# Kernel tuning notes

Hardware: AMD Instinct MI355X
Metric: run time of the kernel (lower is better)

The kernel has to match this reference:

```python
import jax, jax.numpy as jnp
import numpy as np

LN_EPS = 1e-5

def _ln(x, w, b):
    mu = jnp.mean(x, -1, keepdims=True)
    var = jnp.mean((x - mu) ** 2, -1, keepdims=True)
    return (x - mu) / jnp.sqrt(var + LN_EPS) * w + b

def _rot_fwd(x, c, s):
    dh = x.shape[-1] // 2
    r, i = x[..., :dh], x[..., dh:]
    return jnp.concatenate([r * c - i * s, r * s + i * c], axis=-1)

def _rot_inv(x, c, s):
    dh = x.shape[-1] // 2
    r, i = x[..., :dh], x[..., dh:]
    return jnp.concatenate([r * c + i * s, -r * s + i * c], axis=-1)

def _sheaf(x, thetas, alpha, corr_W):
    # causal offsets for window=3
    B, T, d = x.shape
    offsets = [-3, -2, -1, 0]
    lap = jnp.zeros_like(x)
    for idx, delta in enumerate(offsets):
        th = thetas[idx]
        c, s = jnp.cos(th), jnp.sin(th)
        Rx = _rot_fwd(x, c, s)
        if delta == 0:
            x_nb = x
        else:
            ad = -delta
            zeros = jnp.zeros((B, ad, d), dtype=x.dtype)
            x_nb = jnp.concatenate([zeros, x[:, :T - ad, :]], axis=1)
        lap = lap + _rot_inv(Rx - x_nb, c, s)
    out = x - jnp.abs(alpha) * lap
    return out + jnp.einsum('btd,od->bto', out, corr_W)

def _gist_rotation(x, gist_theta, gist_mag, gist_weights, gist_strength, ln_w, ln_b):
    # Scale-1 path: gist_weights present. theta: (B, dh)
    dh = x.shape[-1] // 2
    w = gist_weights[..., None] * gist_mag              # (B, K, 1)
    w = w / (jnp.sum(w, axis=1, keepdims=True) + 1e-8)
    theta = jnp.sum(w * gist_theta, axis=1)             # (B, dh)
    theta = theta * jax.nn.sigmoid(gist_strength)
    c = jnp.cos(theta)[:, None, :]                      # (B, 1, dh)
    s = jnp.sin(theta)[:, None, :]
    r, i = x[..., :dh], x[..., dh:]
    rot = jnp.concatenate([r * c - i * s, r * s + i * c], axis=-1)
    return _ln(rot, ln_w, ln_b)

def _gist_cross_attn(x, gist_theta, gist_mag, Wq, Wk, Wv, Wo, gist_up_W, gist_up_b, n_heads=16):
    B, T, d = x.shape
    K = gist_theta.shape[1]
    dh = d // n_heads
    gist_repr = jnp.einsum('bkf,of->bko', jnp.concatenate([gist_theta, gist_mag], axis=-1), gist_up_W) + gist_up_b  # (B,K,d)
    Q = jnp.einsum('btd,od->bto', x, Wq).reshape(B, T, n_heads, dh).transpose(0, 2, 1, 3)          # (B,H,T,dh)
    Kh = jnp.einsum('bkd,od->bko', gist_repr, Wk).reshape(B, K, n_heads, dh).transpose(0, 2, 1, 3)  # (B,H,K,dh)
    V = jnp.einsum('bkd,od->bko', gist_repr, Wv).reshape(B, K, n_heads, dh).transpose(0, 2, 1, 3)
    scores = jnp.einsum('bhtd,bhkd->bhtk', Q, Kh) / jnp.sqrt(jnp.asarray(dh, x.dtype))
    ctx = jnp.einsum('bhtk,bhkd->bhtd', jax.nn.softmax(scores, axis=-1), V)
    ctx = ctx.transpose(0, 2, 1, 3).reshape(B, T, d)
    return jnp.einsum('btd,od->bto', ctx, Wo)

def _forward(x, gist_theta, gist_mag, gist_weights,
             ln_sheaf_w, ln_sheaf_b, sheaf_thetas, alpha, corr_W,
             ln_gist_w, ln_gist_b, gist_strength, gr_ln_w, gr_ln_b,
             ln_gca_w, ln_gca_b, Wq, Wk, Wv, Wo, gist_up_W, gist_up_b):
    x = x + _sheaf(_ln(x, ln_sheaf_w, ln_sheaf_b), sheaf_thetas, alpha, corr_W)
    xn = _ln(x, ln_gist_w, ln_gist_b)
    x = x + (_gist_rotation(xn, gist_theta, gist_mag, gist_weights, gist_strength, gr_ln_w, gr_ln_b) - xn)
    x = x + _gist_cross_attn(_ln(x, ln_gca_w, ln_gca_b), gist_theta, gist_mag,
                             Wq, Wk, Wv, Wo, gist_up_W, gist_up_b)
    return x

def setup_inputs() -> dict:
    key = jax.random.key(0)
    ks = jax.random.split(key, 16)
    B, T, d, K = 4, 2048, 2048, 16
    dh = d // 2
    scale = 1.0 / np.sqrt(d)
    inp = {
        'x': jax.random.normal(ks[0], (B, T, d), jnp.float32),
        'gist_theta': jax.random.normal(ks[1], (B, K, dh), jnp.float32),
        'gist_mag': jax.random.uniform(ks[2], (B, K, 1), jnp.float32),
        'gist_weights': jax.random.uniform(ks[3], (B, K), jnp.float32),
        'ln_sheaf_w': jnp.ones((d,), jnp.float32),
        'ln_sheaf_b': jnp.zeros((d,), jnp.float32),
        'sheaf_thetas': 0.1 * jax.random.normal(ks[4], (4, dh), jnp.float32),
        'alpha': jnp.asarray(0.15, jnp.float32),
        'corr_W': scale * jax.random.normal(ks[5], (d, d), jnp.float32),
        'ln_gist_w': jnp.ones((d,), jnp.float32),
        'ln_gist_b': jnp.zeros((d,), jnp.float32),
        'gist_strength': jnp.asarray(0.0, jnp.float32),
        'gr_ln_w': jnp.ones((d,), jnp.float32),
        'gr_ln_b': jnp.zeros((d,), jnp.float32),
        'ln_gca_w': jnp.ones((d,), jnp.float32),
        'ln_gca_b': jnp.zeros((d,), jnp.float32),
        'Wq': scale * jax.random.normal(ks[6], (d, d), jnp.float32),
        'Wk': scale * jax.random.normal(ks[7], (d, d), jnp.float32),
        'Wv': scale * jax.random.normal(ks[8], (d, d), jnp.float32),
        'Wo': scale * jax.random.normal(ks[9], (d, d), jnp.float32),
        'gist_up_W': (1.0 / np.sqrt(dh + 1)) * jax.random.normal(ks[10], (d, dh + 1), jnp.float32),
        'gist_up_b': jnp.zeros((d,), jnp.float32),
    }
    return inp

def reference(x, gist_theta, gist_mag, gist_weights,
              ln_sheaf_w, ln_sheaf_b, sheaf_thetas, alpha, corr_W,
              ln_gist_w, ln_gist_b, gist_strength, gr_ln_w, gr_ln_b,
              ln_gca_w, ln_gca_b, Wq, Wk, Wv, Wo, gist_up_W, gist_up_b):
    return _forward(x, gist_theta, gist_mag, gist_weights,
                    ln_sheaf_w, ln_sheaf_b, sheaf_thetas, alpha, corr_W,
                    ln_gist_w, ln_gist_b, gist_strength, gr_ln_w, gr_ln_b,
                    ln_gca_w, ln_gca_b, Wq, Wk, Wv, Wo, gist_up_W, gist_up_b)
```

## Files before the change

kernel.cpp:

```cpp
#include <hip/hip_runtime.h>
#include <hip/hip_bf16.h>

typedef unsigned short u16;
typedef unsigned int   u32;

using frag_ab = __attribute__((ext_vector_type(8))) short;
using frag_cd = __attribute__((ext_vector_type(4))) float;

__device__ __forceinline__ float bf2f(u16 u) {
    union { u32 i; float f; } v; v.i = ((u32)u) << 16; return v.f;
}
__device__ __forceinline__ u16 f2bf(float f) {
    __hip_bfloat16 h = __float2bfloat16(f);
    u16 u; __builtin_memcpy(&u, &h, 2); return u;
}
__device__ __forceinline__ float lo2f(u32 u) { union { u32 i; float f; } v; v.i = u << 16; return v.f; }
__device__ __forceinline__ float hi2f(u32 u) { union { u32 i; float f; } v; v.i = u & 0xffff0000u; return v.f; }
__device__ __forceinline__ void unpack8(uint4 v, float* f) {
    f[0]=lo2f(v.x); f[1]=hi2f(v.x); f[2]=lo2f(v.y); f[3]=hi2f(v.y);
    f[4]=lo2f(v.z); f[5]=hi2f(v.z); f[6]=lo2f(v.w); f[7]=hi2f(v.w);
}
__device__ __forceinline__ void load4f(const u16* p, float* f) {
    ushort4 v = *reinterpret_cast<const ushort4*>(p);
    f[0]=bf2f(v.x); f[1]=bf2f(v.y); f[2]=bf2f(v.z); f[3]=bf2f(v.w);
}
__device__ __forceinline__ void store4bf(u16* p, const float* f) {
    ushort4 v; v.x=f2bf(f[0]); v.y=f2bf(f[1]); v.z=f2bf(f[2]); v.w=f2bf(f[3]);
    *reinterpret_cast<ushort4*>(p) = v;
}
__device__ __forceinline__ u32 pack2(float a, float b) {
    return (u32)f2bf(a) | ((u32)f2bf(b) << 16);
}

__device__ __forceinline__ void gld16(const u16* g, u16* l) {
    __builtin_amdgcn_global_load_lds(
        (const __attribute__((address_space(1))) u32*)g,
        (__attribute__((address_space(3))) u32*)l, 16, 0, 0);
}

__device__ __forceinline__ u32 ldsaddr(const u16* p) {
    return (u32)(uintptr_t)(const __attribute__((address_space(3))) u16*)p;
}

__device__ __forceinline__ frag_ab dsread16(u32 a) {
    frag_ab r;
    asm volatile("ds_read_b128 %0, %1" : "=v"(r) : "v"(a));
    return r;
}

__device__ __forceinline__ void block_reduce2(float& s, float& ss, float* red) {
    #pragma unroll
    for (int off = 32; off > 0; off >>= 1) {
        s  += __shfl_down(s, off, 64);
        ss += __shfl_down(ss, off, 64);
    }
    int wv = threadIdx.x >> 6, ln = threadIdx.x & 63;
    if (ln == 0) { red[wv*2] = s; red[wv*2+1] = ss; }
    __syncthreads();
    s  = red[0] + red[2] + red[4] + red[6];
    ss = red[1] + red[3] + red[5] + red[7];
    __syncthreads();
}

__global__ __launch_bounds__(256) void convert_kernel(
    const float* __restrict__ in, u16* __restrict__ out, int n4)
{
    int i = blockIdx.x * 256 + threadIdx.x;
    if (i < n4) {
        float4 v = reinterpret_cast<const float4*>(in)[i];
        ushort4 o; o.x=f2bf(v.x); o.y=f2bf(v.y); o.z=f2bf(v.z); o.w=f2bf(v.w);
        reinterpret_cast<ushort4*>(out)[i] = o;
    }
}

__global__ __launch_bounds__(256) void apad_kernel(
    const float* __restrict__ gth, const float* __restrict__ gmag,
    u16* __restrict__ Abuf)
{
    const int r = blockIdx.x;
    const int tid = threadIdx.x;
    for (int c0 = tid*4; c0 < 1056; c0 += 1024) {
        float f[4];
        #pragma unroll
        for (int i = 0; i < 4; ++i) {
            int c = c0 + i;
            f[i] = (c < 1024) ? gth[(size_t)r*1024 + c] : (c == 1024 ? gmag[r] : 0.f);
        }
        store4bf(Abuf + (size_t)r*1056 + c0, f);
    }
}

__global__ __launch_bounds__(256) void wpad_kernel(
    const float* __restrict__ upW, u16* __restrict__ Bbuf)
{
    const int r = blockIdx.x;
    const int tid = threadIdx.x;
    for (int c0 = tid*4; c0 < 1056; c0 += 1024) {
        float f[4];
        #pragma unroll
        for (int i = 0; i < 4; ++i) {
            int c = c0 + i;
            f[i] = (c < 1025) ? upW[(size_t)r*1025 + c] : 0.f;
        }
        store4bf(Bbuf + (size_t)r*1056 + c0, f);
    }
}

__global__ __launch_bounds__(256) void setup_kernel(
    const float* __restrict__ sheaf_th, const float* __restrict__ gth,
    const float* __restrict__ gmag, const float* __restrict__ gwts,
    const float* __restrict__ strength, float* __restrict__ sheaf_cs,
    float* __restrict__ gist_cs)
{
    int bx = blockIdx.x, tid = threadIdx.x;
    if (bx < 4) {
        for (int j = tid; j < 1024; j += 256) {
            float th = sheaf_th[bx*1024 + j];
            sheaf_cs[bx*1024 + j]        = cosf(th);
            sheaf_cs[4096 + bx*1024 + j] = sinf(th);
        }
    } else {
        int b = bx - 4;
        float w[16], wsum = 0.f;
        #pragma unroll
        for (int k = 0; k < 16; ++k) {
            w[k] = gwts[b*16+k] * gmag[b*16+k];
            wsum += w[k];
        }
        float inv = 1.f / (wsum + 1e-8f);
        float sig = 1.f / (1.f + expf(-strength[0]));
        for (int j = tid; j < 1024; j += 256) {
            float th = 0.f;
            #pragma unroll
            for (int k = 0; k < 16; ++k)
                th += w[k] * inv * gth[(size_t)(b*16+k)*1024 + j];
            th *= sig;
            gist_cs[b*1024 + j]        = cosf(th);
            gist_cs[4096 + b*1024 + j] = sinf(th);
        }
    }
}

__global__ __launch_bounds__(256) void ln_kernel(
    const float* __restrict__ in, const float* __restrict__ w,
    const float* __restrict__ b, u16* __restrict__ out)
{
    __shared__ float red[8];
    const size_t base = (size_t)blockIdx.x * 2048;
    const int e0 = threadIdx.x * 8;
    float x[8];
    *reinterpret_cast<float4*>(&x[0]) = *reinterpret_cast<const float4*>(in + base + e0);
    *reinterpret_cast<float4*>(&x[4]) = *reinterpret_cast<const float4*>(in + base + e0 + 4);
    float s = 0.f, ss = 0.f;
    #pragma unroll
    for (int i = 0; i < 8; ++i) { s += x[i]; ss += x[i]*x[i]; }
    block_reduce2(s, ss, red);
    const float mu = s * (1.f/2048.f);
    const float rin = rsqrtf(ss * (1.f/2048.f) - mu*mu + 1e-5f);
    float wv[8], bv[8];
    *reinterpret_cast<float4*>(&wv[0]) = *reinterpret_cast<const float4*>(w + e0);
    *reinterpret_cast<float4*>(&wv[4]) = *reinterpret_cast<const float4*>(w + e0 + 4);
    *reinterpret_cast<float4*>(&bv[0]) = *reinterpret_cast<const float4*>(b + e0);
    *reinterpret_cast<float4*>(&bv[4]) = *reinterpret_cast<const float4*>(b + e0 + 4);
    float o[8];
    #pragma unroll
    for (int i = 0; i < 8; ++i) o[i] = (x[i]-mu)*rin*wv[i] + bv[i];
    uint4 st = { pack2(o[0],o[1]), pack2(o[2],o[3]), pack2(o[4],o[5]), pack2(o[6],o[7]) };
    *reinterpret_cast<uint4*>(out + base + e0) = st;
}

__global__ __launch_bounds__(256) void sheaf_kernel(
    const u16* __restrict__ x1, const float* __restrict__ scs,
    const float* __restrict__ alpha_p, u16* __restrict__ pre)
{
    const int row = blockIdx.x;
    const int t = row & 2047;
    const int j0 = threadIdx.x * 4;
    const size_t base = (size_t)row * 2048;
    const float a = fabsf(alpha_p[0]);

    float xr[4], xi[4];
    load4f(x1 + base + j0, xr);
    load4f(x1 + base + 1024 + j0, xi);
    float lr[4], li[4];
    #pragma unroll
    for (int m = 0; m < 4; ++m) { lr[m] = 4.f*xr[m]; li[m] = 4.f*xi[m]; }

    #pragma unroll
    for (int idx = 0; idx < 4; ++idx) {
        const int sh = 3 - idx;
        if (t >= sh) {
            const float4 c4 = *reinterpret_cast<const float4*>(&scs[idx*1024 + j0]);
            const float4 s4 = *reinterpret_cast<const float4*>(&scs[4096 + idx*1024 + j0]);
            float c[4] = {c4.x, c4.y, c4.z, c4.w};
            float sn[4] = {s4.x, s4.y, s4.z, s4.w};
            float yr[4], yi[4];
            load4f(x1 + base - (size_t)sh*2048 + j0, yr);
            load4f(x1 + base - (size_t)sh*2048 + 1024 + j0, yi);
            #pragma unroll
            for (int m = 0; m < 4; ++m) {
                lr[m] -= yr[m]*c[m] + yi[m]*sn[m];
                li[m] -= yi[m]*c[m] - yr[m]*sn[m];
            }
        }
    }
    float pr[4], pi[4];
    #pragma unroll
    for (int m = 0; m < 4; ++m) { pr[m] = xr[m] - a*lr[m]; pi[m] = xi[m] - a*li[m]; }
    store4bf(pre + base + j0, pr);
    store4bf(pre + base + 1024 + j0, pi);
}

__global__ __launch_bounds__(256) void stage2_kernel(
    const u16* __restrict__ xA, const float* __restrict__ gcs,
    const float* __restrict__ lgw, const float* __restrict__ lgb,
    const float* __restrict__ grw, const float* __restrict__ grb,
    const float* __restrict__ gcaw, const float* __restrict__ gcab,
    u16* __restrict__ xB, u16* __restrict__ x2)
{
    __shared__ float red[8];
    const int row = blockIdx.x;
    const int b = row >> 11;
    const int j0 = threadIdx.x * 4;
    const size_t base = (size_t)row * 2048;

    float ar[4], ai[4];
    load4f(xA + base + j0, ar);
    load4f(xA + base + 1024 + j0, ai);

    float s = 0.f, ss = 0.f;
    #pragma unroll
    for (int m = 0; m < 4; ++m) { s += ar[m]+ai[m]; ss += ar[m]*ar[m] + ai[m]*ai[m]; }
    block_reduce2(s, ss, red);
    float mu = s * (1.f/2048.f);
    float rin = rsqrtf(ss * (1.f/2048.f) - mu*mu + 1e-5f);

    float w0[4], b0[4], w1[4], b1[4];
    *reinterpret_cast<float4*>(w0) = *reinterpret_cast<const float4*>(lgw + j0);
    *reinterpret_cast<float4*>(b0) = *reinterpret_cast<const float4*>(lgb + j0);
    *reinterpret_cast<float4*>(w1) = *reinterpret_cast<const float4*>(lgw + 1024 + j0);
    *reinterpret_cast<float4*>(b1) = *reinterpret_cast<const float4*>(lgb + 1024 + j0);
    float xnr[4], xni[4];
    #pragma unroll
    for (int m = 0; m < 4; ++m) {
        xnr[m] = (ar[m]-mu)*rin*w0[m] + b0[m];
        xni[m] = (ai[m]-mu)*rin*w1[m] + b1[m];
    }

    const float4 c4 = *reinterpret_cast<const float4*>(&gcs[b*1024 + j0]);
    const float4 s4 = *reinterpret_cast<const float4*>(&gcs[4096 + b*1024 + j0]);
    float c[4] = {c4.x, c4.y, c4.z, c4.w};
    float sn[4] = {s4.x, s4.y, s4.z, s4.w};
    float rr[4], ri[4];
    #pragma unroll
    for (int m = 0; m < 4; ++m) {
        rr[m] = xnr[m]*c[m] - xni[m]*sn[m];
        ri[m] = xnr[m]*sn[m] + xni[m]*c[m];
    }

    s = 0.f; ss = 0.f;
    #pragma unroll
    for (int m = 0; m < 4; ++m) { s += rr[m]+ri[m]; ss += rr[m]*rr[m] + ri[m]*ri[m]; }
    block_reduce2(s, ss, red);
    float mu2 = s * (1.f/2048.f);
    float rin2 = rsqrtf(ss * (1.f/2048.f) - mu2*mu2 + 1e-5f);

    *reinterpret_cast<float4*>(w0) = *reinterpret_cast<const float4*>(grw + j0);
    *reinterpret_cast<float4*>(b0) = *reinterpret_cast<const float4*>(grb + j0);
    *reinterpret_cast<float4*>(w1) = *reinterpret_cast<const float4*>(grw + 1024 + j0);
    *reinterpret_cast<float4*>(b1) = *reinterpret_cast<const float4*>(grb + 1024 + j0);
    float br[4], bi[4];
    #pragma unroll
    for (int m = 0; m < 4; ++m) {
        float gr_ = (rr[m]-mu2)*rin2*w0[m] + b0[m];
        float gi_ = (ri[m]-mu2)*rin2*w1[m] + b1[m];
        br[m] = ar[m] - xnr[m] + gr_;
        bi[m] = ai[m] - xni[m] + gi_;
    }
    store4bf(xB + base + j0, br);
    store4bf(xB + base + 1024 + j0, bi);

    s = 0.f; ss = 0.f;
    #pragma unroll
    for (int m = 0; m < 4; ++m) { s += br[m]+bi[m]; ss += br[m]*br[m] + bi[m]*bi[m]; }
    block_reduce2(s, ss, red);
    float mu3 = s * (1.f/2048.f);
    float rin3 = rsqrtf(ss * (1.f/2048.f) - mu3*mu3 + 1e-5f);

    *reinterpret_cast<float4*>(w0) = *reinterpret_cast<const float4*>(gcaw + j0);
    *reinterpret_cast<float4*>(b0) = *reinterpret_cast<const float4*>(gcab + j0);
    *reinterpret_cast<float4*>(w1) = *reinterpret_cast<const float4*>(gcaw + 1024 + j0);
    *reinterpret_cast<float4*>(b1) = *reinterpret_cast<const float4*>(gcab + 1024 + j0);
    float o0[4], o1[4];
    #pragma unroll
    for (int m = 0; m < 4; ++m) {
        o0[m] = (br[m]-mu3)*rin3*w0[m] + b0[m];
        o1[m] = (bi[m]-mu3)*rin3*w1[m] + b1[m];
    }
    store4bf(x2 + base + j0, o0);
    store4bf(x2 + base + 1024 + j0, o1);
}

__global__ __launch_bounds__(256) void attn_kernel(
    const u16* __restrict__ Q, const u16* __restrict__ KV,
    u16* __restrict__ ctx)
{
    const int wv = threadIdx.x >> 6;
    const int lane = threadIdx.x & 63;
    const int tg = blockIdx.x * 4 + wv;
    const int b = tg >> 11;
    const size_t base = (size_t)tg * 2048 + lane * 32;

    float q[32];
    #pragma unroll
    for (int c = 0; c < 4; ++c)
        unpack8(*reinterpret_cast<const uint4*>(Q + base + c*8), &q[c*8]);

    float sc[16];
    #pragma unroll
    for (int k = 0; k < 16; ++k) {
        const u16* kr = KV + (size_t)(b*16 + k) * 4096 + lane*32;
        float p = 0.f;
        #pragma unroll
        for (int c = 0; c < 4; ++c) {
            float kv8[8]; unpack8(*reinterpret_cast<const uint4*>(kr + c*8), kv8);
            #pragma unroll
            for (int e = 0; e < 8; ++e) p += q[c*8+e] * kv8[e];
        }
        sc[k] = p;
    }
    #pragma unroll
    for (int k = 0; k < 16; ++k) {
        sc[k] += __shfl_xor(sc[k], 1, 64);
        sc[k] += __shfl_xor(sc[k], 2, 64);
        sc[k] *= 0.08838834764831845f;
    }
    float m = sc[0];
    #pragma unroll
    for (int k = 1; k < 16; ++k) m = fmaxf(m, sc[k]);
    float sum = 0.f;
    #pragma unroll
    for (int k = 0; k < 16; ++k) { sc[k] = expf(sc[k]-m); sum += sc[k]; }
    const float inv = 1.f / sum;

    float o[32];
    #pragma unroll
    for (int e = 0; e < 32; ++e) o[e] = 0.f;
    #pragma unroll
    for (int k = 0; k < 16; ++k) {
        const float p = sc[k] * inv;
        const u16* vr = KV + (size_t)(b*16 + k) * 4096 + 2048 + lane*32;
        #pragma unroll
        for (int c = 0; c < 4; ++c) {
            float v8[8]; unpack8(*reinterpret_cast<const uint4*>(vr + c*8), v8);
            #pragma unroll
            for (int e = 0; e < 8; ++e) o[c*8+e] += p * v8[e];
        }
    }
    #pragma unroll
    for (int c = 0; c < 4; ++c) {
        uint4 st = { pack2(o[c*8+0],o[c*8+1]), pack2(o[c*8+2],o[c*8+3]),
                     pack2(o[c*8+4],o[c*8+5]), pack2(o[c*8+6],o[c*8+7]) };
        *reinterpret_cast<uint4*>(ctx + base + c*8) = st;
    }
}

#define BM 128
#define BN 128
#define BK 32

template<int OUTMODE>
__global__ __launch_bounds__(256) void gemm_bt_kernel(
    const u16* __restrict__ A, const u16* __restrict__ B,
    void* __restrict__ Cv, const float* __restrict__ addf,
    const u16* __restrict__ addb, const float* __restrict__ biasN,
    int M, int N, int K)
{
    __shared__ u16 As[2][8*512];
    __shared__ u16 Bs[2][8*512];

    const int tid = threadIdx.x;
    const int lane = tid & 63;
    const int wave = tid >> 6;
    const int wm = wave >> 1;
    const int wn = wave & 1;
    const int row0 = blockIdx.y * BM;
    const int col0 = blockIdx.x * BN;

    frag_cd acc[4][4] = {};

    const int srow   = lane >> 2;
    const int schunk = (lane & 3) ^ ((lane >> 3) & 3);
    const int scol   = schunk * 8;
    const int s0 = wave, s1 = wave + 4;

    int ra0 = row0 + s0*16 + srow; if (ra0 >= M) ra0 = M - 1;
    int ra1 = row0 + s1*16 + srow; if (ra1 >= M) ra1 = M - 1;
    const u16* gA0 = A + (size_t)ra0 * K + scol;
    const u16* gA1 = A + (size_t)ra1 * K + scol;
    const u16* gB0 = B + (size_t)(col0 + s0*16 + srow) * K + scol;
    const u16* gB1 = B + (size_t)(col0 + s1*16 + srow) * K + scol;

    const int fr = lane & 15;
    const int fq8 = lane >> 4;
    const int fslot = (4*fr + (fq8 ^ ((fr >> 1) & 3))) * 8;

    const int nsteps = K / BK;
    int ts = 0, te = nsteps;
    if (OUTMODE == 2) {
        ts = (nsteps * (int)blockIdx.z) / (int)gridDim.z;
        te = (nsteps * ((int)blockIdx.z + 1)) / (int)gridDim.z;
    }

    gld16(gA0 + ts*BK, &As[0][s0*512]);
    gld16(gA1 + ts*BK, &As[0][s1*512]);
    gld16(gB0 + ts*BK, &Bs[0][s0*512]);
    gld16(gB1 + ts*BK, &Bs[0][s1*512]);
    __syncthreads();

    int cur = 0;
    for (int t = ts; t < te; ++t) {
        if (t + 1 < te) {
            const int kt = (t + 1) * BK;
            gld16(gA0 + kt, &As[cur^1][s0*512]);
            gld16(gA1 + kt, &As[cur^1][s1*512]);
            gld16(gB0 + kt, &Bs[cur^1][s0*512]);
            gld16(gB1 + kt, &Bs[cur^1][s1*512]);
        }

        frag_ab af[4], bf_[4];
        #pragma unroll
        for (int i = 0; i < 4; ++i)
            af[i] = *reinterpret_cast<const frag_ab*>(&As[cur][(wm*4 + i)*512 + fslot]);
        #pragma unroll
        for (int j = 0; j < 4; ++j)
            bf_[j] = *reinterpret_cast<const frag_ab*>(&Bs[cur][(wn*4 + j)*512 + fslot]);
        #pragma unroll
        for (int i = 0; i < 4; ++i)
            #pragma unroll
            for (int j = 0; j < 4; ++j)
                acc[i][j] = __builtin_amdgcn_mfma_f32_16x16x32_bf16(af[i], bf_[j], acc[i][j], 0, 0, 0);

        __syncthreads();
        cur ^= 1;
    }

    float* Pz = (OUTMODE == 2)
        ? reinterpret_cast<float*>(Cv) + (size_t)blockIdx.z * M * N : nullptr;

    #pragma unroll
    for (int i = 0; i < 4; ++i) {
        #pragma unroll
        for (int j = 0; j < 4; ++j) {
            #pragma unroll
            for (int r = 0; r < 4; ++r) {
                const int grow = row0 + wm*64 + i*16 + (lane >> 4) * 4 + r;
                const int gcol = col0 + wn*64 + j*16 + (lane & 15);
                if (grow < M) {
                    const size_t idx = (size_t)grow * N + gcol;
                    float v = acc[i][j][r];
                    if (OUTMODE == 2) {
                        Pz[idx] = v;
                    } else {
                        if (addf) v += addf[idx];
                        if (addb) v += bf2f(addb[idx]);
                        if (biasN) v += biasN[gcol];
                        if (OUTMODE == 1) reinterpret_cast<float*>(Cv)[idx] = v;
                        else              reinterpret_cast<u16*>(Cv)[idx] = f2bf(v);
                    }
                }
            }
        }
    }
}

__global__ __launch_bounds__(256) void ksum_kernel(
    const float* __restrict__ part, int nz, int n4, int N,
    const float* __restrict__ biasN, u16* __restrict__ out)
{
    int i = blockIdx.x * 256 + threadIdx.x;
    if (i >= n4) return;
    const float4* p4 = reinterpret_cast<const float4*>(part);
    float4 s = p4[i];
    for (int z = 1; z < nz; ++z) {
        float4 t = p4[i + (size_t)z * n4];
        s.x += t.x; s.y += t.y; s.z += t.z; s.w += t.w;
    }
    if (biasN) {
        int col = (i * 4) % N;
        s.x += biasN[col]; s.y += biasN[col+1]; s.z += biasN[col+2]; s.w += biasN[col+3];
    }
    ushort4 o; o.x=f2bf(s.x); o.y=f2bf(s.y); o.z=f2bf(s.z); o.w=f2bf(s.w);
    reinterpret_cast<ushort4*>(out)[i] = o;
}

template<int OUTF32>
__global__ __launch_bounds__(512, 2) void gemm256_kernel(
    const u16* __restrict__ A, const u16* __restrict__ B,
    void* __restrict__ Cv, const float* __restrict__ addf,
    const u16* __restrict__ addb, const float* __restrict__ biasN,
    int M, int N, int K)
{
    extern __shared__ u16 lds[];
    u16* Abase = lds;
    u16* Bbase = lds + 32768;

    const int tid  = threadIdx.x;
    const int lane = tid & 63;
    const int wave = tid >> 6;
    const int wm   = wave >> 2;
    const int wn   = wave & 3;
    const int row0 = blockIdx.y * 256;
    const int col0 = blockIdx.x * 256;

    const int srow = lane >> 2;
    const int scol = ((lane & 3) ^ ((lane >> 3) & 3)) * 8;

    const u16* pA = A + (size_t)(row0 + wave*16 + srow) * K + scol;
    const u16* pB = B + (size_t)(col0 + wave*16 + srow) * K + scol;
    const size_t h128 = (size_t)128 * K;

    const int ldsW = wave * 1024;

    const int fr = lane & 15;
    const int fq8 = lane >> 4;
    const int fByte = (4*fr + (fq8 ^ ((fr >> 1) & 3))) * 16;

    const u32 uA = ldsaddr(Abase) + (u32)(wm * 16384) + (u32)fByte;
    const u32 uB = ldsaddr(Bbase) + (u32)((wn >> 1) * 16384 + (wn & 1) * 8192) + (u32)fByte;

    frag_cd acc[8][4] = {};
    frag_ab bfr[4][2];
    frag_ab afr[2][2];

#define STAGE256(SRC, DSTOFF, KT)                                   \
    gld16((SRC) + (KT),      (DSTOFF) + ldsW);                      \
    gld16((SRC) + (KT) + 32, (DSTOFF) + ldsW + 512);

    STAGE256(pB,        Bbase + 0*8192, 0);
    STAGE256(pB + h128, Bbase + 1*8192, 0);
    STAGE256(pA,        Abase + 0*8192, 0);
    STAGE256(pA + h128, Abase + 1*8192, 0);
    STAGE256(pB,        Bbase + 2*8192, 64);
    STAGE256(pB + h128, Bbase + 3*8192, 64);
    asm volatile("s_waitcnt vmcnt(4)" ::: "memory");
    __builtin_amdgcn_s_barrier();

    const int NI = K >> 7;
    for (int i = 0; i < NI; ++i) {
        const int t1k = i*128 + 64;
        int t2k = i*128 + 128; if (t2k >= K) t2k = K - 64;
        int t3k = i*128 + 192; if (t3k >= K) t3k = K - 64;

        #pragma unroll
        for (int p = 0; p < 8; ++p) {
            const int q = p & 3;
            const int bufc = p >> 2;

            if (q == 0) {
                #pragma unroll
                for (int n = 0; n < 4; ++n)
                    #pragma unroll
                    for (int ks = 0; ks < 2; ++ks)
                        bfr[n][ks] = dsread16(uB + (u32)(bufc*32768 + (n*2 + ks)*1024));
            }
            #pragma unroll
            for (int r = 0; r < 2; ++r)
                #pragma unroll
                for (int ks = 0; ks < 2; ++ks)
                    afr[r][ks] = dsread16(uA + (u32)(bufc*32768 + ((2*q + r)*2 + ks)*1024));

            switch (p) {
                case 0: STAGE256(pA,        Abase + 2*8192, t1k); break;
                case 1: STAGE256(pA + h128, Abase + 3*8192, t1k); break;
                case 2: STAGE256(pB,        Bbase + 0*8192, t2k); break;
                case 3: STAGE256(pB + h128, Bbase + 1*8192, t2k); break;
                case 4: STAGE256(pA,        Abase + 0*8192, t2k); break;
                case 5: STAGE256(pA + h128, Abase + 1*8192, t2k); break;
                case 6: STAGE256(pB,        Bbase + 2*8192, t3k); break;
                case 7: STAGE256(pB + h128, Bbase + 3*8192, t3k); break;
            }
            if (q == 0) asm volatile("s_waitcnt lgkmcnt(8)" ::: "memory");
            if (q == 3) asm volatile("s_waitcnt vmcnt(4)" ::: "memory");
            __builtin_amdgcn_s_barrier();
            asm volatile("s_waitcnt lgkmcnt(0)" ::: "memory");
            __builtin_amdgcn_sched_barrier(0);

            __builtin_amdgcn_s_setprio(1);
            #pragma unroll
            for (int ks = 0; ks < 2; ++ks)
                #pragma unroll
                for (int r = 0; r < 2; ++r)
                    #pragma unroll
                    for (int n = 0; n < 4; ++n)
                        acc[2*q + r][n] = __builtin_amdgcn_mfma_f32_16x16x32_bf16(
                            afr[r][ks], bfr[n][ks], acc[2*q + r][n], 0, 0, 0);
            __builtin_amdgcn_s_setprio(0);
            __builtin_amdgcn_s_barrier();
        }
    }
    asm volatile("s_waitcnt vmcnt(0)" ::: "memory");
#undef STAGE256

    #pragma unroll
    for (int m = 0; m < 8; ++m) {
        #pragma unroll
        for (int n = 0; n < 4; ++n) {
            #pragma unroll
            for (int r = 0; r < 4; ++r) {
                const int grow = row0 + wm*128 + m*16 + (lane >> 4) * 4 + r;
                const int gcol = col0 + wn*64 + n*16 + (lane & 15);
                const size_t idx = (size_t)grow * N + gcol;
                float v = acc[m][n][r];
                if (addf) v += addf[idx];
                if (addb) v += bf2f(addb[idx]);
                if (biasN) v += biasN[gcol];
                if (OUTF32) reinterpret_cast<float*>(Cv)[idx] = v;
                else        reinterpret_cast<u16*>(Cv)[idx] = f2bf(v);
            }
        }
    }
}

extern "C" void kernel_launch(void* const* d_in, const int* in_sizes, int n_in,
                              void* d_out, int out_size, void* d_ws, size_t ws_size,
                              hipStream_t stream)
{
    const float* x          = (const float*)d_in[0];
    const float* gist_theta = (const float*)d_in[1];
    const float* gist_mag   = (const float*)d_in[2];
    const float* gist_wts   = (const float*)d_in[3];
    const float* ln_sheaf_w = (const float*)d_in[4];
    const float* ln_sheaf_b = (const float*)d_in[5];
    const float* sheaf_th   = (const float*)d_in[6];
    const float* alpha      = (const float*)d_in[7];
    const float* corr_W     = (const float*)d_in[8];
    const float* ln_gist_w  = (const float*)d_in[9];
    const float* ln_gist_b  = (const float*)d_in[10];
    const float* strength   = (const float*)d_in[11];
    const float* gr_w       = (const float*)d_in[12];
    const float* gr_b       = (const float*)d_in[13];
    const float* gca_w      = (const float*)d_in[14];
    const float* gca_b      = (const float*)d_in[15];
    const float* Wq         = (const float*)d_in[16];
    const float* Wk         = (const float*)d_in[17];
    const float* Wv         = (const float*)d_in[18];
    const float* Wo         = (const float*)d_in[19];
    const float* up_W       = (const float*)d_in[20];
    const float* up_b       = (const float*)d_in[21];
    float* out = (float*)d_out;

    static bool attr_done = false;
    if (!attr_done) {
        hipFuncSetAttribute((const void*)&gemm256_kernel<0>,
                            hipFuncAttributeMaxDynamicSharedMemorySize, 131072);
        hipFuncSetAttribute((const void*)&gemm256_kernel<1>,
                            hipFuncAttributeMaxDynamicSharedMemorySize, 131072);
        attr_done = true;
    }

    char* w = (char*)d_ws;
    const size_t BIG = (size_t)4 * 2048 * 2048 * sizeof(u16);
    u16* wA = (u16*)(w);
    u16* wB = (u16*)(w + BIG);
    u16* wC = (u16*)(w + 2*BIG);
    u16* wslot = (u16*)(w + 3*BIG);
    char* small = w + 3*BIG + (size_t)2048*2048*sizeof(u16);
    float* sheaf_cs = (float*)(small);
    float* gist_cs  = (float*)(small + 32768);
    u16* repr = (u16*)(small + 65536);
    u16* KV   = repr + 64*2048;
    float* part = (float*)((char*)KV + (size_t)64*4096*sizeof(u16));
    const size_t part_bytes = (size_t)8 * 64 * 4096 * sizeof(float);
    const bool ksplit = ws_size >= (size_t)((char*)part - w) + part_bytes;

    const int W4 = 2048*2048/4;
    const dim3 gBig256(2048/256, 8192/256), gKV(32, 1), gRepr(16, 1);

    setup_kernel<<<8, 256, 0, stream>>>(sheaf_th, gist_theta, gist_mag, gist_wts,
                                        strength, sheaf_cs, gist_cs);

    apad_kernel<<<64, 256, 0, stream>>>(gist_theta, gist_mag, wC);
    wpad_kernel<<<2048, 256, 0, stream>>>(up_W, wslot);
    if (ksplit) {
        gemm_bt_kernel<2><<<dim3(16,1,4), 256, 0, stream>>>(wC, wslot, part,
                                                 nullptr, nullptr, nullptr, 64, 2048, 1056);
        ksum_kernel<<<(64*2048/4 + 255)/256, 256, 0, stream>>>(part, 4, 64*2048/4, 2048,
                                                 up_b, repr);
    } else {
        gemm_bt_kernel<0><<<gRepr, 256, 0, stream>>>(wC, wslot, repr, nullptr, nullptr, up_b,
                                                     64, 2048, 1056);
    }

    convert_kernel<<<4096, 256, 0, stream>>>(Wk, wB, W4);
    convert_kernel<<<4096, 256, 0, stream>>>(Wv, wB + (size_t)2048*2048, W4);
    if (ksplit) {
        gemm_bt_kernel<2><<<dim3(32,1,8), 256, 0, stream>>>(repr, wB, part,
                                                 nullptr, nullptr, nullptr, 64, 4096, 2048);
        ksum_kernel<<<(64*4096/4 + 255)/256, 256, 0, stream>>>(part, 8, 64*4096/4, 4096,
                                                 nullptr, KV);
    } else {
        gemm_bt_kernel<0><<<gKV, 256, 0, stream>>>(repr, wB, KV, nullptr, nullptr, nullptr,
                                                   64, 4096, 2048);
    }

    ln_kernel<<<8192, 256, 0, stream>>>(x, ln_sheaf_w, ln_sheaf_b, wA);
    sheaf_kernel<<<8192, 256, 0, stream>>>(wA, sheaf_cs, alpha, wB);

    convert_kernel<<<4096, 256, 0, stream>>>(corr_W, wslot, W4);
    gemm256_kernel<0><<<gBig256, 512, 131072, stream>>>(wB, wslot, wA, x, wB, nullptr,
                                                8192, 2048, 2048);
    stage2_kernel<<<8192, 256, 0, stream>>>(wA, gist_cs, ln_gist_w, ln_gist_b,
                                            gr_w, gr_b, gca_w, gca_b,
                                            wC, wA);
    convert_kernel<<<4096, 256, 0, stream>>>(Wq, wslot, W4);
    gemm256_kernel<0><<<gBig256, 512, 131072, stream>>>(wA, wslot, wB, nullptr, nullptr, nullptr,
                                                8192, 2048, 2048);
    attn_kernel<<<2048, 256, 0, stream>>>(wB, KV, wA);
    convert_kernel<<<4096, 256, 0, stream>>>(Wo, wslot, W4);
    gemm256_kernel<1><<<gBig256, 512, 131072, stream>>>(wA, wslot, (void*)out, nullptr, wC, nullptr,
                                                8192, 2048, 2048);
}
```

Baseline: 647.2 us.

## Remap GEMM blocks across XCDs and batch weight conversions into separate slots

The 256x256 GEMM now remaps its block index so consecutive tiles are spread across the 8 XCDs in chunks, which is meant to improve L2 reuse of A and B tiles. All weight fp32-to-bf16 conversions are batched into two multi-matrix kernels at the start and written to dedicated workspace slots when the workspace is large enough, cutting launch count and serial convert steps. The small GEMM also gets an occupancy hint in its launch bounds. The cost is more workspace, and the fallback handling is fragile: when there is room for the extra slots but not the padding buffer, the padded weights are written past the checked region and a buffer that was never filled with them is read.

```diff
diff --git a/kernel.cpp b/kernel.cpp
--- a/kernel.cpp
+++ b/kernel.cpp
@@ -71,6 +71,33 @@
         ushort4 o; o.x=f2bf(v.x); o.y=f2bf(v.y); o.z=f2bf(v.z); o.w=f2bf(v.w);
         reinterpret_cast<ushort4*>(out)[i] = o;
     }
+}
+
+__global__ __launch_bounds__(256) void convert2_kernel(
+    const float* __restrict__ s0, const float* __restrict__ s1,
+    u16* __restrict__ d0, u16* __restrict__ d1, int n4)
+{
+    int i = blockIdx.x * 256 + threadIdx.x;
+    if (i >= n4) return;
+    const float* s = blockIdx.y ? s1 : s0;
+    u16*         d = blockIdx.y ? d1 : d0;
+    float4 v = reinterpret_cast<const float4*>(s)[i];
+    ushort4 o; o.x=f2bf(v.x); o.y=f2bf(v.y); o.z=f2bf(v.z); o.w=f2bf(v.w);
+    reinterpret_cast<ushort4*>(d)[i] = o;
+}
+
+__global__ __launch_bounds__(256) void convert3_kernel(
+    const float* __restrict__ s0, const float* __restrict__ s1,
+    const float* __restrict__ s2,
+    u16* __restrict__ d0, u16* __restrict__ d1, u16* __restrict__ d2, int n4)
+{
+    int i = blockIdx.x * 256 + threadIdx.x;
+    if (i >= n4) return;
+    const float* s = blockIdx.y == 0 ? s0 : (blockIdx.y == 1 ? s1 : s2);
+    u16*         d = blockIdx.y == 0 ? d0 : (blockIdx.y == 1 ? d1 : d2);
+    float4 v = reinterpret_cast<const float4*>(s)[i];
+    ushort4 o; o.x=f2bf(v.x); o.y=f2bf(v.y); o.z=f2bf(v.z); o.w=f2bf(v.w);
+    reinterpret_cast<ushort4*>(d)[i] = o;
 }
 
 __global__ __launch_bounds__(256) void apad_kernel(
@@ -370,7 +397,7 @@
 #define BK 32
 
 template<int OUTMODE>
-__global__ __launch_bounds__(256) void gemm_bt_kernel(
+__global__ __launch_bounds__(256, 4) void gemm_bt_kernel(
     const u16* __restrict__ A, const u16* __restrict__ B,
     void* __restrict__ Cv, const float* __restrict__ addf,
     const u16* __restrict__ addb, const float* __restrict__ biasN,
@@ -510,8 +537,16 @@
     const int wave = tid >> 6;
     const int wm   = wave >> 2;
     const int wn   = wave & 3;
-    const int row0 = blockIdx.y * 256;
-    const int col0 = blockIdx.x * 256;
+
+    int id = (int)(blockIdx.y * gridDim.x + blockIdx.x);
+    {
+        const int nwg = (int)(gridDim.x * gridDim.y);
+        if ((nwg & 7) == 0) id = (id & 7) * (nwg >> 3) + (id >> 3);
+    }
+    const int bx = id % (int)gridDim.x;
+    const int by = id / (int)gridDim.x;
+    const int row0 = by * 256;
+    const int col0 = bx * 256;
 
     const int srow = lane >> 2;
     const int scol = ((lane & 3) ^ ((lane >> 3) & 3)) * 8;
@@ -672,7 +707,12 @@
     u16* KV   = repr + 64*2048;
     float* part = (float*)((char*)KV + (size_t)64*4096*sizeof(u16));
     const size_t part_bytes = (size_t)8 * 64 * 4096 * sizeof(float);
-    const bool ksplit = ws_size >= (size_t)((char*)part - w) + part_bytes;
+    char* after_part = (char*)part + part_bytes;
+    const bool ksplit = ws_size >= (size_t)(after_part - w);
+
+    u16* wslot2 = (u16*)after_part;
+    u16* wslot3 = wslot2 + (size_t)2048*2048;
+    const bool roomy = ws_size >= (size_t)((char*)(wslot3 + (size_t)2048*2048) - w);
 
     const int W4 = 2048*2048/4;
     const dim3 gBig256(2048/256, 8192/256), gKV(32, 1), gRepr(16, 1);
@@ -680,20 +720,29 @@
     setup_kernel<<<8, 256, 0, stream>>>(sheaf_th, gist_theta, gist_mag, gist_wts,
                                         strength, sheaf_cs, gist_cs);
 
+    if (roomy) {
+        convert3_kernel<<<dim3(4096,3), 256, 0, stream>>>(corr_W, Wq, Wo,
+                                                          wslot, wslot2, wslot3, W4);
+    }
+    convert2_kernel<<<dim3(4096,2), 256, 0, stream>>>(Wk, Wv,
+                                                      wB, wB + (size_t)2048*2048, W4);
+
     apad_kernel<<<64, 256, 0, stream>>>(gist_theta, gist_mag, wC);
-    wpad_kernel<<<2048, 256, 0, stream>>>(up_W, wslot);
+    wpad_kernel<<<2048, 256, 0, stream>>>(up_W, roomy ? (u16*)((char*)wslot3 + (size_t)2048*2048*2) : wslot);
+    const bool padroom = ws_size >= (size_t)((char*)(wslot3 + (size_t)2048*2048) - w)
+                         + (size_t)2048*1056*sizeof(u16);
+    u16* padbuf = (roomy && padroom) ? (u16*)((char*)(wslot3 + (size_t)2048*2048)) : wslot;
+
     if (ksplit) {
-        gemm_bt_kernel<2><<<dim3(16,1,4), 256, 0, stream>>>(wC, wslot, part,
+        gemm_bt_kernel<2><<<dim3(16,1,4), 256, 0, stream>>>(wC, padbuf, part,
                                                  nullptr, nullptr, nullptr, 64, 2048, 1056);
         ksum_kernel<<<(64*2048/4 + 255)/256, 256, 0, stream>>>(part, 4, 64*2048/4, 2048,
                                                  up_b, repr);
     } else {
-        gemm_bt_kernel<0><<<gRepr, 256, 0, stream>>>(wC, wslot, repr, nullptr, nullptr, up_b,
+        gemm_bt_kernel<0><<<gRepr, 256, 0, stream>>>(wC, padbuf, repr, nullptr, nullptr, up_b,
                                                      64, 2048, 1056);
     }
 
-    convert_kernel<<<4096, 256, 0, stream>>>(Wk, wB, W4);
-    convert_kernel<<<4096, 256, 0, stream>>>(Wv, wB + (size_t)2048*2048, W4);
     if (ksplit) {
         gemm_bt_kernel<2><<<dim3(32,1,8), 256, 0, stream>>>(repr, wB, part,
                                                  nullptr, nullptr, nullptr, 64, 4096, 2048);
@@ -707,17 +756,22 @@
     ln_kernel<<<8192, 256, 0, stream>>>(x, ln_sheaf_w, ln_sheaf_b, wA);
     sheaf_kernel<<<8192, 256, 0, stream>>>(wA, sheaf_cs, alpha, wB);
 
-    convert_kernel<<<4096, 256, 0, stream>>>(corr_W, wslot, W4);
+    if (!roomy || padbuf == wslot)
+        convert_kernel<<<4096, 256, 0, stream>>>(corr_W, wslot, W4);
     gemm256_kernel<0><<<gBig256, 512, 131072, stream>>>(wB, wslot, wA, x, wB, nullptr,
                                                 8192, 2048, 2048);
     stage2_kernel<<<8192, 256, 0, stream>>>(wA, gist_cs, ln_gist_w, ln_gist_b,
                                             gr_w, gr_b, gca_w, gca_b,
                                             wC, wA);
-    convert_kernel<<<4096, 256, 0, stream>>>(Wq, wslot, W4);
-    gemm256_kernel<0><<<gBig256, 512, 131072, stream>>>(wA, wslot, wB, nullptr, nullptr, nullptr,
+    u16* qslot = roomy ? wslot2 : wslot;
+    if (!roomy)
+        convert_kernel<<<4096, 256, 0, stream>>>(Wq, wslot, W4);
+    gemm256_kernel<0><<<gBig256, 512, 131072, stream>>>(wA, qslot, wB, nullptr, nullptr, nullptr,
                                                 8192, 2048, 2048);
     attn_kernel<<<2048, 256, 0, stream>>>(wB, KV, wA);
-    convert_kernel<<<4096, 256, 0, stream>>>(Wo, wslot, W4);
-    gemm256_kernel<1><<<gBig256, 512, 131072, stream>>>(wA, wslot, (void*)out, nullptr, wC, nullptr,
+    u16* oslot = roomy ? wslot3 : wslot;
+    if (!roomy)
+        convert_kernel<<<4096, 256, 0, stream>>>(Wo, wslot, W4);
+    gemm256_kernel<1><<<gBig256, 512, 131072, stream>>>(wA, oslot, (void*)out, nullptr, wC, nullptr,
                                                 8192, 2048, 2048);
 }
```

Measured after the change: 633.2 us. 1.02x faster.
